# Kernel optimization log

Measured on AMD Instinct MI355X. Metric: run time of the kernel, lower is better.

Reference implementation:

```python
import jax, jax.numpy as jnp
import numpy as np

WS = 8   # window size
NH = 8   # num heads


def layernorm(x, g, b, eps=1e-5):
    m = jnp.mean(x, axis=-1, keepdims=True)
    v = jnp.var(x, axis=-1, keepdims=True)
    return (x - m) * jax.lax.rsqrt(v + eps) * g + b


def setup_inputs() -> dict:
    key = jax.random.key(0)
    ks = jax.random.split(key, 8)
    B, C, H, W = 16, 256, 64, 64
    s = 0.02
    inp = {
        "x": jax.random.normal(ks[0], (B, C, H, W), jnp.float32),
        "norm1_g": jnp.ones((C,), jnp.float32),
        "norm1_b": jnp.zeros((C,), jnp.float32),
        "qkv_w": jax.random.normal(ks[1], (3 * C, C), jnp.float32) * s,
        "qkv_b": jnp.zeros((3 * C,), jnp.float32),
        "rel_bias_table": jax.random.normal(ks[2], ((2 * WS - 1) ** 2, NH), jnp.float32) * s,
        "proj_w": jax.random.normal(ks[3], (C, C), jnp.float32) * s,
        "proj_b": jnp.zeros((C,), jnp.float32),
        "norm2_g": jnp.ones((C,), jnp.float32),
        "norm2_b": jnp.zeros((C,), jnp.float32),
        "fc1_w": jax.random.normal(ks[4], (4 * C, C), jnp.float32) * s,
        "fc1_b": jnp.zeros((4 * C,), jnp.float32),
        "fc2_w": jax.random.normal(ks[5], (C, 4 * C), jnp.float32) * s,
        "fc2_b": jnp.zeros((C,), jnp.float32),
    }
    # relative position index (Swin standard), shape (WS*WS, WS*WS), int constant
    coords = np.stack(np.meshgrid(np.arange(WS), np.arange(WS), indexing="ij")).reshape(2, -1)
    rel = (coords[:, :, None] - coords[:, None, :]).transpose(1, 2, 0)
    rel[:, :, 0] += WS - 1
    rel[:, :, 1] += WS - 1
    rel[:, :, 0] *= 2 * WS - 1
    inp["rel_index"] = jnp.asarray(rel.sum(-1), jnp.int32)
    return inp


def reference(x, norm1_g, norm1_b, qkv_w, qkv_b, rel_bias_table, proj_w, proj_b,
              norm2_g, norm2_b, fc1_w, fc1_b, fc2_w, fc2_b, rel_index):
    B, C, H, W = x.shape
    N = WS * WS
    hd = C // NH
    scale = hd ** -0.5

    xs = jnp.transpose(x, (0, 2, 3, 1)).reshape(B, H * W, C)  # b (h w) c
    shortcut = xs

    y = layernorm(xs, norm1_g, norm1_b).reshape(B, H, W, C)
    # window partition -> (B*nW, N, C); shift_size = 0 (default), no cyclic shift / mask
    y = y.reshape(B, H // WS, WS, W // WS, WS, C).transpose(0, 1, 3, 2, 4, 5).reshape(-1, N, C)

    qkv = (y @ qkv_w.T + qkv_b).reshape(-1, N, 3, NH, hd).transpose(2, 0, 3, 1, 4)
    q, k, v = qkv[0], qkv[1], qkv[2]  # each (nW*B, NH, N, hd)

    attn = jnp.einsum("whnd,whmd->whnm", q * scale, k)
    bias = rel_bias_table[rel_index].transpose(2, 0, 1)  # (NH, N, N)
    attn = jax.nn.softmax(attn + bias[None], axis=-1)
    out = jnp.einsum("whnm,whmd->whnd", attn, v).transpose(0, 2, 1, 3).reshape(-1, N, C)
    out = out @ proj_w.T + proj_b

    # window reverse -> (B, H*W, C)
    out = out.reshape(B, H // WS, W // WS, WS, WS, C).transpose(0, 1, 3, 2, 4, 5).reshape(B, H * W, C)

    xs = shortcut + out
    h = layernorm(xs, norm2_g, norm2_b)
    h = jax.nn.gelu(h @ fc1_w.T + fc1_b, approximate=False) @ fc2_w.T + fc2_b
    xs = xs + h

    return jnp.transpose(xs.reshape(B, H, W, C), (0, 3, 1, 2))
```

## Files before the change

### kernel.cpp

```cpp
#include <hip/hip_runtime.h>

typedef unsigned short u16;
typedef __attribute__((ext_vector_type(8))) short short8;
typedef __attribute__((ext_vector_type(4))) float f32x4;

#define MFMA16(a, b, c) __builtin_amdgcn_mfma_f32_16x16x32_bf16((a), (b), (c), 0, 0, 0)
#define WAITV(N) asm volatile("s_waitcnt vmcnt(" #N ")" ::: "memory")
#define BARS() __builtin_amdgcn_s_barrier()
#define MFENCE() asm volatile("" ::: "memory")

__device__ __forceinline__ u16 f2b(float f) {
  unsigned b = __float_as_uint(f);
  b += 0x7FFFu + ((b >> 16) & 1u);
  return (u16)(b >> 16);
}

__device__ __forceinline__ void gload_lds16(const void* g, void* l) {
  __builtin_amdgcn_global_load_lds((const __attribute__((address_space(1))) void*)g,
                                   (__attribute__((address_space(3))) void*)l, 16, 0, 0);
}

__device__ __forceinline__ float fast_gelu(float x) {
  const float u = x * 0.70710678118654752f;
  const float au = fabsf(u);
  float d = 1.f + 0.3275911f * au;
  float tt;
  asm("v_rcp_f32 %0, %1" : "=v"(tt) : "v"(d));
  float p = 1.061405429f * tt - 1.453152027f;
  p = p * tt + 1.421413741f;
  p = p * tt - 0.284496736f;
  p = p * tt + 0.254829592f;
  p = p * tt;
  const float e = __expf(-u * u);
  const float erf_au = 1.f - p * e;
  return 0.5f * x * (1.f + copysignf(erf_au, x));
}

__global__ __launch_bounds__(256) void prep_kernel(
    const float* __restrict__ qkv_w, const float* __restrict__ proj_w,
    const float* __restrict__ fc1_w, const float* __restrict__ fc2_w,
    const float* __restrict__ tbl, const int* __restrict__ ridx,
    u16* __restrict__ wqkv, u16* __restrict__ wproj, u16* __restrict__ wfc1,
    u16* __restrict__ wfc2, float* __restrict__ bfull) {
  int i = blockIdx.x * 256 + threadIdx.x;
  if (i < 196608) {
    wqkv[i] = f2b(qkv_w[i]);
  } else if (i < 262144) {
    wproj[i - 196608] = f2b(proj_w[i - 196608]);
  } else if (i < 524288) {
    wfc1[i - 262144] = f2b(fc1_w[i - 262144]);
  } else if (i < 786432) {
    wfc2[i - 524288] = f2b(fc2_w[i - 524288]);
  } else {
    int j = i - 786432;
    int hm = j >> 12, nm = j & 4095;
    bfull[j] = tbl[ridx[nm] * 8 + hm];
  }
}

__global__ __launch_bounds__(256) void ln1_win_kernel(const float* __restrict__ x,
                                                      const float* __restrict__ g,
                                                      const float* __restrict__ b,
                                                      u16* __restrict__ y) {
  __shared__ float red[2][4][64];
  const int bh = blockIdx.x;
  const int bb = bh >> 6, h = bh & 63;
  const int w = threadIdx.x & 63, cg = threadIdx.x >> 6;
  const float* xp = x + (size_t)bb * 1048576 + (size_t)h * 64 + w;
  float vals[64];
  float s = 0.f, ss = 0.f;
#pragma unroll
  for (int j = 0; j < 64; ++j) {
    float v = xp[(size_t)(cg * 64 + j) * 4096];
    vals[j] = v;
    s += v;
    ss += v * v;
  }
  red[0][cg][w] = s;
  red[1][cg][w] = ss;
  __syncthreads();
  const float S = red[0][0][w] + red[0][1][w] + red[0][2][w] + red[0][3][w];
  const float Q = red[1][0][w] + red[1][1][w] + red[1][2][w] + red[1][3][w];
  const float m = S * (1.f / 256.f);
  const float rstd = rsqrtf(Q * (1.f / 256.f) - m * m + 1e-5f);
  const int win = bb * 64 + ((h >> 3) << 3) + (w >> 3);
  const int tok = ((h & 7) << 3) + (w & 7);
  u16* yp = y + (size_t)win * 16384 + tok * 256 + cg * 64;
#pragma unroll
  for (int jj = 0; jj < 8; ++jj) {
    short8 o;
#pragma unroll
    for (int q = 0; q < 8; ++q) {
      const int c64 = jj * 8 + q;
      const int c = cg * 64 + c64;
      o[q] = (short)f2b((vals[c64] - m) * rstd * g[c] + b[c]);
    }
    *(short8*)&yp[jj * 8] = o;
  }
}

template <int EPI, int KT, int NNT>
__global__ __launch_bounds__(256, 3) void gemm_bt(const u16* __restrict__ A,
                                                  const u16* __restrict__ W,
                                                  const float* __restrict__ bias,
                                                  u16* __restrict__ outh,
                                                  float* __restrict__ outf,
                                                  const float* __restrict__ aux) {
  constexpr int NTK = KT >> 5;
  constexpr int NC = NNT * 128;
  __shared__ __align__(16) u16 As[3][4096];
  __shared__ __align__(16) u16 Bs[3][4096];
  const int xcd = blockIdx.x & 7, ii = blockIdx.x >> 3;
  const int mt = xcd * 64 + ii / NNT;
  const int nt = ii % NNT;
  const int tid = threadIdx.x;
  const int wv = tid >> 6, lane = tid & 63;
  const int wr = (wv >> 1) << 6;
  const int wc = (wv & 1) << 6;
  const int lrow4 = lane >> 2;
  const int srcslot = (((lane & 3) ^ ((lane >> 3) & 3)) << 3);
  const int lr = lane & 15, lg = lane >> 4;
  const int kq = ((lg ^ ((lr >> 1) & 3)) << 3);
  f32x4 acc[4][4];
#pragma unroll
  for (int mi = 0; mi < 4; ++mi)
#pragma unroll
    for (int ni = 0; ni < 4; ++ni) acc[mi][ni] = (f32x4){0.f, 0.f, 0.f, 0.f};
  const u16* Ab = A + (size_t)mt * 128 * KT;
  const u16* Wb = W + (size_t)nt * 128 * KT;

#define STG(BF, T)                                                                      \
  {                                                                                     \
    const int kt_ = (T) << 5;                                                           \
    _Pragma("unroll") for (int i_ = 0; i_ < 2; ++i_) {                                  \
      const int row_ = i_ * 64 + wv * 16 + lrow4;                                       \
      const int lo_ = i_ * 2048 + wv * 512;                                             \
      gload_lds16(Ab + (size_t)row_ * KT + kt_ + srcslot, &As[BF][lo_]);                \
      gload_lds16(Wb + (size_t)row_ * KT + kt_ + srcslot, &Bs[BF][lo_]);                \
    }                                                                                   \
  }
#define CMPT(BF)                                                                        \
  {                                                                                     \
    short8 a_[4], b_[4];                                                                \
    _Pragma("unroll") for (int mi = 0; mi < 4; ++mi)                                    \
        a_[mi] = *(const short8*)&As[BF][(wr + mi * 16 + lr) * 32 + kq];                \
    _Pragma("unroll") for (int ni = 0; ni < 4; ++ni)                                    \
        b_[ni] = *(const short8*)&Bs[BF][(wc + ni * 16 + lr) * 32 + kq];                \
    _Pragma("unroll") for (int mi = 0; mi < 4; ++mi)                                    \
        _Pragma("unroll") for (int ni = 0; ni < 4; ++ni)                                \
            acc[mi][ni] = MFMA16(a_[mi], b_[ni], acc[mi][ni]);                          \
  }

  STG(0, 0);
  STG(1, 1);
  STG(2, 2);
  int rr = 0;
  for (int t = 0; t < NTK; ++t) {
    if (t + 2 < NTK) {
      WAITV(8);
    } else if (t + 1 < NTK) {
      WAITV(4);
    } else {
      WAITV(0);
    }
    BARS();
    MFENCE();
    CMPT(rr);
    MFENCE();
    BARS();
    if (t + 3 < NTK) STG(rr, t + 3);
    rr = (rr == 2) ? 0 : rr + 1;
  }
#undef STG
#undef CMPT

  const int row0 = mt * 128 + wr + lg * 4;
  const int col0 = nt * 128 + wc + lr;

  if constexpr (EPI == 0) {
#pragma unroll
    for (int mi = 0; mi < 4; ++mi)
#pragma unroll
      for (int ni = 0; ni < 4; ++ni) {
        const int col = col0 + ni * 16;
        const int which = col >> 8, cc = col & 255;
        const int head = cc >> 5, hd = cc & 31;
        u16* dst = outh + (size_t)which * 16777216ull;
        const float scl = (which == 0) ? 0.17677669529663689f : 1.0f;
        const float bv = bias[col];
#pragma unroll
        for (int r = 0; r < 4; ++r) {
          const int row = row0 + mi * 16 + r;
          const int win = row >> 6, tk = row & 63;
          dst[(((size_t)(win * 8 + head) << 6) + tk) * 32 + hd] =
              f2b((acc[mi][ni][r] + bv) * scl);
        }
      }
  } else if constexpr (EPI == 1) {
#pragma unroll
    for (int mi = 0; mi < 4; ++mi)
#pragma unroll
      for (int ni = 0; ni < 4; ++ni) {
        const int col = col0 + ni * 16;
        const float bv = bias[col];
#pragma unroll
        for (int r = 0; r < 4; ++r) {
          const int row = row0 + mi * 16 + r;
          const int win = row >> 6, tk = row & 63;
          const int bb = win >> 6;
          const int h = (((win >> 3) & 7) << 3) + (tk >> 3);
          const int w = ((win & 7) << 3) + (tk & 7);
          float val = acc[mi][ni][r] + bv +
                      aux[(((size_t)bb * 256 + col) * 64 + h) * 64 + w];
          outf[(size_t)row * 256 + col] = val;
        }
      }
  } else if constexpr (EPI == 2) {
#pragma unroll
    for (int mi = 0; mi < 4; ++mi)
#pragma unroll
      for (int ni = 0; ni < 4; ++ni) {
        const int col = col0 + ni * 16;
        const float bv = bias[col];
#pragma unroll
        for (int r = 0; r < 4; ++r) {
          const int row = row0 + mi * 16 + r;
          outh[(size_t)row * NC + col] = f2b(fast_gelu(acc[mi][ni][r] + bv));
        }
      }
  } else {
#pragma unroll
    for (int mi = 0; mi < 4; ++mi)
#pragma unroll
      for (int ni = 0; ni < 4; ++ni) {
        const int col = col0 + ni * 16;
        const float bv = bias[col];
        const int row = row0 + mi * 16;
        const int win = row >> 6, tk = row & 63;
        const int bb = win >> 6;
        const int h = (((win >> 3) & 7) << 3) + (tk >> 3);
        const int w = ((win & 7) << 3) + (tk & 7);
        f32x4 v;
#pragma unroll
        for (int r = 0; r < 4; ++r)
          v[r] = acc[mi][ni][r] + bv + aux[(size_t)(row + r) * 256 + col];
        *(f32x4*)&outf[(((size_t)bb * 256 + col) * 64 + h) * 64 + w] = v;
      }
  }
}

__global__ __launch_bounds__(64) void attn_kernel(const u16* __restrict__ qkv,
                                                  const float* __restrict__ biasf,
                                                  u16* __restrict__ aout) {
  __shared__ __align__(16) u16 sqk[5120];
  __shared__ __align__(16) u16 vt[2304];
  u16* qs = sqk;
  u16* ks = sqk + 2560;
  u16* pp = sqk;
  const int wh = blockIdx.x;
  const int head = wh & 7;
  const int win = wh >> 3;
  const int lane = threadIdx.x;
  const int lr = lane & 15, lg = lane >> 4;
  const u16* qg = qkv + (size_t)wh * 2048;
  const u16* kg = qkv + 16777216ull + (size_t)wh * 2048;
  const u16* vg = qkv + 33554432ull + (size_t)wh * 2048;
#pragma unroll
  for (int i = 0; i < 4; ++i) {
    int ch = i * 64 + lane;
    int r = ch >> 2, qo = (ch & 3) * 8;
    *(short8*)&qs[r * 40 + qo] = *(const short8*)&qg[r * 32 + qo];
    *(short8*)&ks[r * 40 + qo] = *(const short8*)&kg[r * 32 + qo];
  }
  {
    short8 v0 = *(const short8*)&vg[(size_t)lane * 32];
    short8 v1 = *(const short8*)&vg[(size_t)lane * 32 + 8];
    short8 v2 = *(const short8*)&vg[(size_t)lane * 32 + 16];
    short8 v3 = *(const short8*)&vg[(size_t)lane * 32 + 24];
#pragma unroll
    for (int j = 0; j < 8; ++j) {
      vt[j * 72 + lane] = (u16)v0[j];
      vt[(8 + j) * 72 + lane] = (u16)v1[j];
      vt[(16 + j) * 72 + lane] = (u16)v2[j];
      vt[(24 + j) * 72 + lane] = (u16)v3[j];
    }
  }
  __syncthreads();
  f32x4 sf[4][4];
#pragma unroll
  for (int mi = 0; mi < 4; ++mi)
#pragma unroll
    for (int ni = 0; ni < 4; ++ni) sf[mi][ni] = (f32x4){0.f, 0.f, 0.f, 0.f};
  {
    short8 a[4], bq[4];
#pragma unroll
    for (int mi = 0; mi < 4; ++mi) a[mi] = *(const short8*)&qs[(mi * 16 + lr) * 40 + lg * 8];
#pragma unroll
    for (int ni = 0; ni < 4; ++ni) bq[ni] = *(const short8*)&ks[(ni * 16 + lr) * 40 + lg * 8];
#pragma unroll
    for (int mi = 0; mi < 4; ++mi)
#pragma unroll
      for (int ni = 0; ni < 4; ++ni) sf[mi][ni] = MFMA16(a[mi], bq[ni], sf[mi][ni]);
  }
  __syncthreads();
  const float* bh = biasf + (size_t)head * 4096;
#pragma unroll
  for (int mi = 0; mi < 4; ++mi) {
#pragma unroll
    for (int r = 0; r < 4; ++r) {
      const int n = mi * 16 + lg * 4 + r;
      float v0 = sf[mi][0][r] + bh[n * 64 + lr];
      float v1 = sf[mi][1][r] + bh[n * 64 + 16 + lr];
      float v2 = sf[mi][2][r] + bh[n * 64 + 32 + lr];
      float v3 = sf[mi][3][r] + bh[n * 64 + 48 + lr];
      float mx = fmaxf(fmaxf(v0, v1), fmaxf(v2, v3));
      mx = fmaxf(mx, __shfl_xor(mx, 1));
      mx = fmaxf(mx, __shfl_xor(mx, 2));
      mx = fmaxf(mx, __shfl_xor(mx, 4));
      mx = fmaxf(mx, __shfl_xor(mx, 8));
      float e0 = __expf(v0 - mx), e1 = __expf(v1 - mx);
      float e2 = __expf(v2 - mx), e3 = __expf(v3 - mx);
      float sm = e0 + e1 + e2 + e3;
      sm += __shfl_xor(sm, 1);
      sm += __shfl_xor(sm, 2);
      sm += __shfl_xor(sm, 4);
      sm += __shfl_xor(sm, 8);
      const float inv = 1.f / sm;
      pp[n * 72 + lr] = f2b(e0 * inv);
      pp[n * 72 + 16 + lr] = f2b(e1 * inv);
      pp[n * 72 + 32 + lr] = f2b(e2 * inv);
      pp[n * 72 + 48 + lr] = f2b(e3 * inv);
    }
  }
  __syncthreads();
  f32x4 o[4][2];
#pragma unroll
  for (int mi = 0; mi < 4; ++mi)
#pragma unroll
    for (int ni = 0; ni < 2; ++ni) o[mi][ni] = (f32x4){0.f, 0.f, 0.f, 0.f};
#pragma unroll
  for (int kk = 0; kk < 2; ++kk) {
    short8 pa[4], vb[2];
#pragma unroll
    for (int mi = 0; mi < 4; ++mi)
      pa[mi] = *(const short8*)&pp[(mi * 16 + lr) * 72 + kk * 32 + lg * 8];
#pragma unroll
    for (int ni = 0; ni < 2; ++ni)
      vb[ni] = *(const short8*)&vt[(ni * 16 + lr) * 72 + kk * 32 + lg * 8];
#pragma unroll
    for (int mi = 0; mi < 4; ++mi)
#pragma unroll
      for (int ni = 0; ni < 2; ++ni) o[mi][ni] = MFMA16(pa[mi], vb[ni], o[mi][ni]);
  }
  u16* op = aout + (size_t)win * 16384 + head * 32;
#pragma unroll
  for (int mi = 0; mi < 4; ++mi)
#pragma unroll
    for (int ni = 0; ni < 2; ++ni)
#pragma unroll
      for (int r = 0; r < 4; ++r) {
        const int n = mi * 16 + lg * 4 + r;
        op[(size_t)n * 256 + ni * 16 + lr] = f2b(o[mi][ni][r]);
      }
}

__global__ __launch_bounds__(256) void ln2_kernel(const float* __restrict__ xs2,
                                                  const float* __restrict__ g,
                                                  const float* __restrict__ b,
                                                  u16* __restrict__ h2) {
  const int wv = threadIdx.x >> 6, lane = threadIdx.x & 63;
  const size_t row = (size_t)blockIdx.x * 4 + wv;
  const f32x4 xv = *(const f32x4*)&xs2[row * 256 + lane * 4];
  float s = xv[0] + xv[1] + xv[2] + xv[3];
  float q = xv[0] * xv[0] + xv[1] * xv[1] + xv[2] * xv[2] + xv[3] * xv[3];
#pragma unroll
  for (int off = 1; off < 64; off <<= 1) {
    s += __shfl_xor(s, off);
    q += __shfl_xor(q, off);
  }
  const float m = s * (1.f / 256.f);
  const float rstd = rsqrtf(q * (1.f / 256.f) - m * m + 1e-5f);
  const f32x4 gv = *(const f32x4*)&g[lane * 4];
  const f32x4 bv = *(const f32x4*)&b[lane * 4];
  union {
    u16 u[4];
    unsigned long long v;
  } pk;
#pragma unroll
  for (int j = 0; j < 4; ++j) pk.u[j] = f2b((xv[j] - m) * rstd * gv[j] + bv[j]);
  *(unsigned long long*)&h2[row * 256 + lane * 4] = pk.v;
}

extern "C" void kernel_launch(void* const* d_in, const int* in_sizes, int n_in,
                              void* d_out, int out_size, void* d_ws, size_t ws_size,
                              hipStream_t stream) {
  const float* x = (const float*)d_in[0];
  const float* n1g = (const float*)d_in[1];
  const float* n1b = (const float*)d_in[2];
  const float* qkv_w = (const float*)d_in[3];
  const float* qkv_b = (const float*)d_in[4];
  const float* tbl = (const float*)d_in[5];
  const float* proj_w = (const float*)d_in[6];
  const float* proj_b = (const float*)d_in[7];
  const float* n2g = (const float*)d_in[8];
  const float* n2b = (const float*)d_in[9];
  const float* fc1_w = (const float*)d_in[10];
  const float* fc1_b = (const float*)d_in[11];
  const float* fc2_w = (const float*)d_in[12];
  const float* fc2_b = (const float*)d_in[13];
  const int* relidx = (const int*)d_in[14];
  float* outp = (float*)d_out;

  char* w = (char*)d_ws;
  const size_t Mi = 1ull << 20;
  if (ws_size < 237 * Mi) return;
  u16* Y = (u16*)(w + 0);
  u16* qb = (u16*)(w + 32 * Mi);
  u16* aout = (u16*)(w + 0);
  float* xs2 = (float*)(w + 32 * Mi);
  u16* h2 = (u16*)(w + 0);
  u16* h1 = (u16*)(w + 96 * Mi);
  u16* wqkv = (u16*)(w + 224 * Mi);
  u16* wproj = wqkv + 196608;
  u16* wfc1 = wproj + 65536;
  u16* wfc2 = wfc1 + 262144;
  float* bfull = (float*)(w + 224 * Mi + 1572864);

  prep_kernel<<<3200, 256, 0, stream>>>(qkv_w, proj_w, fc1_w, fc2_w, tbl, relidx, wqkv,
                                        wproj, wfc1, wfc2, bfull);
  ln1_win_kernel<<<1024, 256, 0, stream>>>(x, n1g, n1b, Y);
  gemm_bt<0, 256, 6><<<3072, 256, 0, stream>>>(Y, wqkv, qkv_b, qb, nullptr, nullptr);
  attn_kernel<<<8192, 64, 0, stream>>>(qb, bfull, aout);
  gemm_bt<1, 256, 2><<<1024, 256, 0, stream>>>(aout, wproj, proj_b, nullptr, xs2, x);
  ln2_kernel<<<16384, 256, 0, stream>>>(xs2, n2g, n2b, h2);
  gemm_bt<2, 256, 8><<<4096, 256, 0, stream>>>(h2, wfc1, fc1_b, h1, nullptr, nullptr);
  gemm_bt<3, 1024, 2><<<1024, 256, 0, stream>>>(h1, wfc2, fc2_b, nullptr, outp, xs2);
}
```

Measured before the change: 313.1 us.

## Fuse proj GEMM with LN2, enlarge GEMM tiles, store residuals in bf16

LN1 now also writes a bf16 copy of the input in window order, so the proj epilogue no longer does a strided fp32 gather from x. The proj GEMM becomes a 128x256 full-row tile kernel that adds bias and residual, computes LayerNorm2 through a cross-wave reduction, and writes both the bf16 residual and the normalized activations, which removes the separate ln2 kernel and the fp32 xs2 buffer. The other GEMMs move to 512-thread blocks with 256-row tiles for more operand reuse. Keeping the residuals in bf16 cuts memory traffic but lowers precision on the skip path.

```diff
diff --git a/kernel.cpp b/kernel.cpp
--- a/kernel.cpp
+++ b/kernel.cpp
@@ -14,6 +14,7 @@
   b += 0x7FFFu + ((b >> 16) & 1u);
   return (u16)(b >> 16);
 }
+__device__ __forceinline__ float b2f(u16 u) { return __uint_as_float(((unsigned)u) << 16); }
 
 __device__ __forceinline__ void gload_lds16(const void* g, void* l) {
   __builtin_amdgcn_global_load_lds((const __attribute__((address_space(1))) void*)g,
@@ -61,7 +62,8 @@
 __global__ __launch_bounds__(256) void ln1_win_kernel(const float* __restrict__ x,
                                                       const float* __restrict__ g,
                                                       const float* __restrict__ b,
-                                                      u16* __restrict__ y) {
+                                                      u16* __restrict__ y,
+                                                      u16* __restrict__ xsb) {
   __shared__ float red[2][4][64];
   const int bh = blockIdx.x;
   const int bb = bh >> 6, h = bh & 63;
@@ -85,40 +87,41 @@
   const float rstd = rsqrtf(Q * (1.f / 256.f) - m * m + 1e-5f);
   const int win = bb * 64 + ((h >> 3) << 3) + (w >> 3);
   const int tok = ((h & 7) << 3) + (w & 7);
-  u16* yp = y + (size_t)win * 16384 + tok * 256 + cg * 64;
+  const size_t base = (size_t)win * 16384 + tok * 256 + cg * 64;
 #pragma unroll
   for (int jj = 0; jj < 8; ++jj) {
-    short8 o;
+    short8 o, raw;
 #pragma unroll
     for (int q = 0; q < 8; ++q) {
       const int c64 = jj * 8 + q;
       const int c = cg * 64 + c64;
+      raw[q] = (short)f2b(vals[c64]);
       o[q] = (short)f2b((vals[c64] - m) * rstd * g[c] + b[c]);
     }
-    *(short8*)&yp[jj * 8] = o;
+    *(short8*)&y[base + jj * 8] = o;
+    *(short8*)&xsb[base + jj * 8] = raw;
   }
 }
 
 template <int EPI, int KT, int NNT>
-__global__ __launch_bounds__(256, 3) void gemm_bt(const u16* __restrict__ A,
+__global__ __launch_bounds__(512, 4) void gemm256(const u16* __restrict__ A,
                                                   const u16* __restrict__ W,
                                                   const float* __restrict__ bias,
                                                   u16* __restrict__ outh,
                                                   float* __restrict__ outf,
-                                                  const float* __restrict__ aux) {
+                                                  const u16* __restrict__ aux) {
   constexpr int NTK = KT >> 5;
   constexpr int NC = NNT * 128;
-  __shared__ __align__(16) u16 As[3][4096];
+  __shared__ __align__(16) u16 As[3][8192];
   __shared__ __align__(16) u16 Bs[3][4096];
   const int xcd = blockIdx.x & 7, ii = blockIdx.x >> 3;
-  const int mt = xcd * 64 + ii / NNT;
+  const int mt = xcd * 32 + ii / NNT;
   const int nt = ii % NNT;
   const int tid = threadIdx.x;
   const int wv = tid >> 6, lane = tid & 63;
-  const int wr = (wv >> 1) << 6;
-  const int wc = (wv & 1) << 6;
-  const int lrow4 = lane >> 2;
-  const int srcslot = (((lane & 3) ^ ((lane >> 3) & 3)) << 3);
+  const int wm = wv >> 1, wn = wv & 1;
+  const int rowa = tid >> 2;
+  const int esl = (((tid & 3) ^ ((tid >> 3) & 3)) << 3);
   const int lr = lane & 15, lg = lane >> 4;
   const int kq = ((lg ^ ((lr >> 1) & 3)) << 3);
   f32x4 acc[4][4];
@@ -126,26 +129,23 @@
   for (int mi = 0; mi < 4; ++mi)
 #pragma unroll
     for (int ni = 0; ni < 4; ++ni) acc[mi][ni] = (f32x4){0.f, 0.f, 0.f, 0.f};
-  const u16* Ab = A + (size_t)mt * 128 * KT;
+  const u16* Ab = A + (size_t)mt * 256 * KT;
   const u16* Wb = W + (size_t)nt * 128 * KT;
 
 #define STG(BF, T)                                                                      \
   {                                                                                     \
     const int kt_ = (T) << 5;                                                           \
-    _Pragma("unroll") for (int i_ = 0; i_ < 2; ++i_) {                                  \
-      const int row_ = i_ * 64 + wv * 16 + lrow4;                                       \
-      const int lo_ = i_ * 2048 + wv * 512;                                             \
-      gload_lds16(Ab + (size_t)row_ * KT + kt_ + srcslot, &As[BF][lo_]);                \
-      gload_lds16(Wb + (size_t)row_ * KT + kt_ + srcslot, &Bs[BF][lo_]);                \
-    }                                                                                   \
+    gload_lds16(Ab + (size_t)rowa * KT + kt_ + esl, &As[BF][tid * 8]);                  \
+    gload_lds16(Ab + (size_t)(rowa + 128) * KT + kt_ + esl, &As[BF][tid * 8 + 4096]);   \
+    gload_lds16(Wb + (size_t)rowa * KT + kt_ + esl, &Bs[BF][tid * 8]);                  \
   }
 #define CMPT(BF)                                                                        \
   {                                                                                     \
     short8 a_[4], b_[4];                                                                \
     _Pragma("unroll") for (int mi = 0; mi < 4; ++mi)                                    \
-        a_[mi] = *(const short8*)&As[BF][(wr + mi * 16 + lr) * 32 + kq];                \
+        a_[mi] = *(const short8*)&As[BF][(wm * 64 + mi * 16 + lr) * 32 + kq];           \
     _Pragma("unroll") for (int ni = 0; ni < 4; ++ni)                                    \
-        b_[ni] = *(const short8*)&Bs[BF][(wc + ni * 16 + lr) * 32 + kq];                \
+        b_[ni] = *(const short8*)&Bs[BF][(wn * 64 + ni * 16 + lr) * 32 + kq];           \
     _Pragma("unroll") for (int mi = 0; mi < 4; ++mi)                                    \
         _Pragma("unroll") for (int ni = 0; ni < 4; ++ni)                                \
             acc[mi][ni] = MFMA16(a_[mi], b_[ni], acc[mi][ni]);                          \
@@ -157,9 +157,9 @@
   int rr = 0;
   for (int t = 0; t < NTK; ++t) {
     if (t + 2 < NTK) {
-      WAITV(8);
+      WAITV(6);
     } else if (t + 1 < NTK) {
-      WAITV(4);
+      WAITV(3);
     } else {
       WAITV(0);
     }
@@ -174,8 +174,8 @@
 #undef STG
 #undef CMPT
 
-  const int row0 = mt * 128 + wr + lg * 4;
-  const int col0 = nt * 128 + wc + lr;
+  const int row0 = mt * 256 + wm * 64 + lg * 4;
+  const int col0 = nt * 128 + wn * 64 + lr;
 
   if constexpr (EPI == 0) {
 #pragma unroll
@@ -194,25 +194,6 @@
           const int win = row >> 6, tk = row & 63;
           dst[(((size_t)(win * 8 + head) << 6) + tk) * 32 + hd] =
               f2b((acc[mi][ni][r] + bv) * scl);
-        }
-      }
-  } else if constexpr (EPI == 1) {
-#pragma unroll
-    for (int mi = 0; mi < 4; ++mi)
-#pragma unroll
-      for (int ni = 0; ni < 4; ++ni) {
-        const int col = col0 + ni * 16;
-        const float bv = bias[col];
-#pragma unroll
-        for (int r = 0; r < 4; ++r) {
-          const int row = row0 + mi * 16 + r;
-          const int win = row >> 6, tk = row & 63;
-          const int bb = win >> 6;
-          const int h = (((win >> 3) & 7) << 3) + (tk >> 3);
-          const int w = ((win & 7) << 3) + (tk & 7);
-          float val = acc[mi][ni][r] + bv +
-                      aux[(((size_t)bb * 256 + col) * 64 + h) * 64 + w];
-          outf[(size_t)row * 256 + col] = val;
         }
       }
   } else if constexpr (EPI == 2) {
@@ -243,10 +224,129 @@
         f32x4 v;
 #pragma unroll
         for (int r = 0; r < 4; ++r)
-          v[r] = acc[mi][ni][r] + bv + aux[(size_t)(row + r) * 256 + col];
+          v[r] = acc[mi][ni][r] + bv + b2f(aux[(size_t)(row + r) * 256 + col]);
         *(f32x4*)&outf[(((size_t)bb * 256 + col) * 64 + h) * 64 + w] = v;
       }
   }
+}
+
+__global__ __launch_bounds__(512, 4) void proj_ln2(const u16* __restrict__ A,
+                                                   const u16* __restrict__ W,
+                                                   const float* __restrict__ bias,
+                                                   const u16* __restrict__ xsb,
+                                                   const float* __restrict__ g2,
+                                                   const float* __restrict__ b2,
+                                                   u16* __restrict__ xs2b,
+                                                   u16* __restrict__ h2) {
+  __shared__ __align__(16) u16 As[3][4096];
+  __shared__ __align__(16) u16 Bs[3][8192];
+  __shared__ float redS[4][128], redQ[4][128];
+  const int mt = blockIdx.x;
+  const int tid = threadIdx.x;
+  const int wv = tid >> 6, lane = tid & 63;
+  const int wm = wv >> 2, wn = wv & 3;
+  const int rowa = tid >> 2;
+  const int esl = (((tid & 3) ^ ((tid >> 3) & 3)) << 3);
+  const int lr = lane & 15, lg = lane >> 4;
+  const int kq = ((lg ^ ((lr >> 1) & 3)) << 3);
+  f32x4 acc[4][4];
+#pragma unroll
+  for (int mi = 0; mi < 4; ++mi)
+#pragma unroll
+    for (int ni = 0; ni < 4; ++ni) acc[mi][ni] = (f32x4){0.f, 0.f, 0.f, 0.f};
+  const u16* Ab = A + (size_t)mt * 128 * 256;
+
+#define STG(BF, T)                                                                      \
+  {                                                                                     \
+    const int kt_ = (T) << 5;                                                           \
+    gload_lds16(Ab + (size_t)rowa * 256 + kt_ + esl, &As[BF][tid * 8]);                 \
+    gload_lds16(W + (size_t)rowa * 256 + kt_ + esl, &Bs[BF][tid * 8]);                  \
+    gload_lds16(W + (size_t)(rowa + 128) * 256 + kt_ + esl, &Bs[BF][tid * 8 + 4096]);   \
+  }
+#define CMPT(BF)                                                                        \
+  {                                                                                     \
+    short8 a_[4], b_[4];                                                                \
+    _Pragma("unroll") for (int mi = 0; mi < 4; ++mi)                                    \
+        a_[mi] = *(const short8*)&As[BF][(wm * 64 + mi * 16 + lr) * 32 + kq];           \
+    _Pragma("unroll") for (int ni = 0; ni < 4; ++ni)                                    \
+        b_[ni] = *(const short8*)&Bs[BF][(wn * 64 + ni * 16 + lr) * 32 + kq];           \
+    _Pragma("unroll") for (int mi = 0; mi < 4; ++mi)                                    \
+        _Pragma("unroll") for (int ni = 0; ni < 4; ++ni)                                \
+            acc[mi][ni] = MFMA16(a_[mi], b_[ni], acc[mi][ni]);                          \
+  }
+
+  STG(0, 0);
+  STG(1, 1);
+  STG(2, 2);
+  int rr = 0;
+  for (int t = 0; t < 8; ++t) {
+    if (t + 2 < 8) {
+      WAITV(6);
+    } else if (t + 1 < 8) {
+      WAITV(3);
+    } else {
+      WAITV(0);
+    }
+    BARS();
+    MFENCE();
+    CMPT(rr);
+    MFENCE();
+    BARS();
+    if (t + 3 < 8) STG(rr, t + 3);
+    rr = (rr == 2) ? 0 : rr + 1;
+  }
+#undef STG
+#undef CMPT
+
+  const int row0 = mt * 128 + wm * 64 + lg * 4;
+  const int col0 = wn * 64 + lr;
+
+#pragma unroll
+  for (int mi = 0; mi < 4; ++mi)
+#pragma unroll
+    for (int ni = 0; ni < 4; ++ni) {
+      const int col = col0 + ni * 16;
+      const float bv = bias[col];
+#pragma unroll
+      for (int r = 0; r < 4; ++r)
+        acc[mi][ni][r] += bv + b2f(xsb[(size_t)(row0 + mi * 16 + r) * 256 + col]);
+    }
+#pragma unroll
+  for (int mi = 0; mi < 4; ++mi)
+#pragma unroll
+    for (int r = 0; r < 4; ++r) {
+      float s = acc[mi][0][r] + acc[mi][1][r] + acc[mi][2][r] + acc[mi][3][r];
+      float q = acc[mi][0][r] * acc[mi][0][r] + acc[mi][1][r] * acc[mi][1][r] +
+                acc[mi][2][r] * acc[mi][2][r] + acc[mi][3][r] * acc[mi][3][r];
+      s += __shfl_xor(s, 1); q += __shfl_xor(q, 1);
+      s += __shfl_xor(s, 2); q += __shfl_xor(q, 2);
+      s += __shfl_xor(s, 4); q += __shfl_xor(q, 4);
+      s += __shfl_xor(s, 8); q += __shfl_xor(q, 8);
+      if (lr == 0) {
+        const int rl = wm * 64 + mi * 16 + lg * 4 + r;
+        redS[wn][rl] = s;
+        redQ[wn][rl] = q;
+      }
+    }
+  __syncthreads();
+#pragma unroll
+  for (int mi = 0; mi < 4; ++mi)
+#pragma unroll
+    for (int r = 0; r < 4; ++r) {
+      const int rl = wm * 64 + mi * 16 + lg * 4 + r;
+      const float S = redS[0][rl] + redS[1][rl] + redS[2][rl] + redS[3][rl];
+      const float Q = redQ[0][rl] + redQ[1][rl] + redQ[2][rl] + redQ[3][rl];
+      const float m = S * (1.f / 256.f);
+      const float rstd = rsqrtf(Q * (1.f / 256.f) - m * m + 1e-5f);
+      const size_t row = row0 + mi * 16 + r;
+#pragma unroll
+      for (int ni = 0; ni < 4; ++ni) {
+        const int col = col0 + ni * 16;
+        const float v = acc[mi][ni][r];
+        xs2b[row * 256 + col] = f2b(v);
+        h2[row * 256 + col] = f2b((v - m) * rstd * g2[col] + b2[col]);
+      }
+    }
 }
 
 __global__ __launch_bounds__(64) void attn_kernel(const u16* __restrict__ qkv,
@@ -364,33 +464,6 @@
       }
 }
 
-__global__ __launch_bounds__(256) void ln2_kernel(const float* __restrict__ xs2,
-                                                  const float* __restrict__ g,
-                                                  const float* __restrict__ b,
-                                                  u16* __restrict__ h2) {
-  const int wv = threadIdx.x >> 6, lane = threadIdx.x & 63;
-  const size_t row = (size_t)blockIdx.x * 4 + wv;
-  const f32x4 xv = *(const f32x4*)&xs2[row * 256 + lane * 4];
-  float s = xv[0] + xv[1] + xv[2] + xv[3];
-  float q = xv[0] * xv[0] + xv[1] * xv[1] + xv[2] * xv[2] + xv[3] * xv[3];
-#pragma unroll
-  for (int off = 1; off < 64; off <<= 1) {
-    s += __shfl_xor(s, off);
-    q += __shfl_xor(q, off);
-  }
-  const float m = s * (1.f / 256.f);
-  const float rstd = rsqrtf(q * (1.f / 256.f) - m * m + 1e-5f);
-  const f32x4 gv = *(const f32x4*)&g[lane * 4];
-  const f32x4 bv = *(const f32x4*)&b[lane * 4];
-  union {
-    u16 u[4];
-    unsigned long long v;
-  } pk;
-#pragma unroll
-  for (int j = 0; j < 4; ++j) pk.u[j] = f2b((xv[j] - m) * rstd * gv[j] + bv[j]);
-  *(unsigned long long*)&h2[row * 256 + lane * 4] = pk.v;
-}
-
 extern "C" void kernel_launch(void* const* d_in, const int* in_sizes, int n_in,
                               void* d_out, int out_size, void* d_ws, size_t ws_size,
                               hipStream_t stream) {
@@ -417,22 +490,22 @@
   u16* Y = (u16*)(w + 0);
   u16* qb = (u16*)(w + 32 * Mi);
   u16* aout = (u16*)(w + 0);
-  float* xs2 = (float*)(w + 32 * Mi);
-  u16* h2 = (u16*)(w + 0);
-  u16* h1 = (u16*)(w + 96 * Mi);
-  u16* wqkv = (u16*)(w + 224 * Mi);
+  u16* xs2b = (u16*)(w + 0);
+  u16* h2 = (u16*)(w + 32 * Mi);
+  u16* xsb = (u16*)(w + 128 * Mi);
+  u16* h1 = (u16*)(w + 64 * Mi);
+  u16* wqkv = (u16*)(w + 192 * Mi);
   u16* wproj = wqkv + 196608;
   u16* wfc1 = wproj + 65536;
   u16* wfc2 = wfc1 + 262144;
-  float* bfull = (float*)(w + 224 * Mi + 1572864);
+  float* bfull = (float*)(w + 192 * Mi + 1572864);
 
   prep_kernel<<<3200, 256, 0, stream>>>(qkv_w, proj_w, fc1_w, fc2_w, tbl, relidx, wqkv,
                                         wproj, wfc1, wfc2, bfull);
-  ln1_win_kernel<<<1024, 256, 0, stream>>>(x, n1g, n1b, Y);
-  gemm_bt<0, 256, 6><<<3072, 256, 0, stream>>>(Y, wqkv, qkv_b, qb, nullptr, nullptr);
+  ln1_win_kernel<<<1024, 256, 0, stream>>>(x, n1g, n1b, Y, xsb);
+  gemm256<0, 256, 6><<<1536, 512, 0, stream>>>(Y, wqkv, qkv_b, qb, nullptr, nullptr);
   attn_kernel<<<8192, 64, 0, stream>>>(qb, bfull, aout);
-  gemm_bt<1, 256, 2><<<1024, 256, 0, stream>>>(aout, wproj, proj_b, nullptr, xs2, x);
-  ln2_kernel<<<16384, 256, 0, stream>>>(xs2, n2g, n2b, h2);
-  gemm_bt<2, 256, 8><<<4096, 256, 0, stream>>>(h2, wfc1, fc1_b, h1, nullptr, nullptr);
-  gemm_bt<3, 1024, 2><<<1024, 256, 0, stream>>>(h1, wfc2, fc2_b, nullptr, outp, xs2);
-}
+  proj_ln2<<<512, 512, 0, stream>>>(aout, wproj, proj_b, xsb, n2g, n2b, xs2b, h2);
+  gemm256<2, 256, 8><<<2048, 512, 0, stream>>>(h2, wfc1, fc1_b, h1, nullptr, nullptr);
+  gemm256<3, 1024, 2><<<512, 512, 0, stream>>>(h1, wfc2, fc2_b, nullptr, outp, xs2b);
+}
```

New measurement: 348.0 us. 11.1% more time.
